# Optimization experiments

Measured on AMD Instinct MI355X. Metric: run time of the kernel, lower is better.

Reference implementation:

```python
import jax, jax.numpy as jnp
import numpy as np

NEG_SLOPE = 0.2  # PyG GATConv default


def gat_conv(x, edge_index, W, a_src, a_dst, bias):
    """Single-head PyG-style GATConv (eval mode, add_self_loops=True)."""
    N = x.shape[0]
    h = x @ W  # [N, F_out]
    # add self loops
    loops = jnp.arange(N, dtype=edge_index.dtype)
    src = jnp.concatenate([edge_index[0], loops])  # [E+N]
    dst = jnp.concatenate([edge_index[1], loops])
    # per-edge attention logits: a_src . h_j + a_dst . h_i  (j=src, i=dst)
    alpha_s = h @ a_src  # [N]
    alpha_d = h @ a_dst  # [N]
    e = jax.nn.leaky_relu(alpha_s[src] + alpha_d[dst], NEG_SLOPE)  # [E+N]
    # segment softmax over incoming edges of each dst node
    m = jax.ops.segment_max(e, dst, num_segments=N)
    ex = jnp.exp(e - m[dst])
    denom = jax.ops.segment_sum(ex, dst, num_segments=N)
    alpha = ex / denom[dst]  # [E+N]
    # weighted scatter-aggregate of source features
    out = jax.ops.segment_sum(h[src] * alpha[:, None], dst, num_segments=N)
    return out + bias


def setup_inputs() -> dict:
    key = jax.random.key(0)
    ks = jax.random.split(key, 12)
    N, E = 100000, 3200000
    Fin, H, Fout = 128, 32, 32
    x = jax.random.normal(ks[0], (N, Fin), dtype=jnp.float32)
    edge_index = jax.random.randint(ks[1], (2, E), 0, N, dtype=jnp.int64)
    s = 1.0 / np.sqrt(Fin)
    W1 = jax.random.uniform(ks[2], (Fin, H), jnp.float32, -s, s)
    a1s = jax.random.uniform(ks[3], (H,), jnp.float32, -s, s)
    a1d = jax.random.uniform(ks[4], (H,), jnp.float32, -s, s)
    b1 = jnp.zeros((H,), jnp.float32)
    s2 = 1.0 / np.sqrt(H)
    W2 = jax.random.uniform(ks[5], (H, H), jnp.float32, -s2, s2)
    a2s = jax.random.uniform(ks[6], (H,), jnp.float32, -s2, s2)
    a2d = jax.random.uniform(ks[7], (H,), jnp.float32, -s2, s2)
    b2 = jnp.zeros((H,), jnp.float32)
    Wf = jax.random.uniform(ks[8], (H, Fout), jnp.float32, -s2, s2)
    bf = jax.random.uniform(ks[9], (Fout,), jnp.float32, -s2, s2)
    return {"x": x, "edge_index": edge_index, "W1": W1, "a1s": a1s, "a1d": a1d,
            "b1": b1, "W2": W2, "a2s": a2s, "a2d": a2d, "b2": b2,
            "Wf": Wf, "bf": bf}


def reference(x, edge_index, W1, a1s, a1d, b1, W2, a2s, a2d, b2, Wf, bf):
    h = jax.nn.relu(gat_conv(x, edge_index, W1, a1s, a1d, b1))
    h = jax.nn.relu(gat_conv(h, edge_index, W2, a2s, a2d, b2))
    return h @ Wf + bf
```

## Files before the change

### kernel.cpp

```cpp
#include <hip/hip_runtime.h>

#define NEG_SLOPE 0.2f
#define BK_LOG 9
#define BK_NODES (1 << BK_LOG)
#define TILE_EPT 24
#define TILE_E (256 * TILE_EPT)

typedef __attribute__((ext_vector_type(8))) short bf8_t;
typedef __attribute__((ext_vector_type(4))) float f32x4;

__device__ __forceinline__ float leaky(float v) { return v > 0.0f ? v : NEG_SLOPE * v; }

__device__ __forceinline__ unsigned short f2bf(float f) {
    unsigned u = __float_as_uint(f);
    u += 0x7fffu + ((u >> 16) & 1u);
    return (unsigned short)(u >> 16);
}
__device__ __forceinline__ float bf2f(unsigned short h) {
    return __uint_as_float(((unsigned)h) << 16);
}

__device__ __forceinline__ int scan256_excl(int v, int* tmp) {
    int t = threadIdx.x;
    tmp[t] = v;
    __syncthreads();
    for (int d = 1; d < 256; d <<= 1) {
        int x = (t >= d) ? tmp[t - d] : 0;
        __syncthreads();
        tmp[t] += x;
        __syncthreads();
    }
    int r = tmp[t] - v;
    __syncthreads();
    return r;
}

__device__ __forceinline__ void wsplit_body(int blk, int tid,
                                            const float* __restrict__ W,
                                            unsigned short* __restrict__ wh,
                                            unsigned short* __restrict__ wl, int K) {
    int idx = blk * 256 + tid;
    int KT = K >> 5;
    if (idx >= KT * 128) return;
    int lane = idx & 63;
    int nt = (idx >> 6) & 1;
    int kt = idx >> 7;
    int q = lane >> 4, c = lane & 15;
#pragma unroll
    for (int j = 0; j < 8; ++j) {
        int k = kt * 32 + q * 8 + j;
        int n = nt * 16 + c;
        float w = W[k * 32 + n];
        unsigned short hi = f2bf(w);
        wh[idx * 8 + j] = hi;
        wl[idx * 8 + j] = f2bf(w - bf2f(hi));
    }
}

__global__ __launch_bounds__(256) void k_prep(
    const float* __restrict__ W1, unsigned short* __restrict__ wh1, unsigned short* __restrict__ wl1,
    int* __restrict__ bcnt)
{
    int b = blockIdx.x, t = threadIdx.x;
    if (b < 2) wsplit_body(b, t, W1, wh1, wl1, 128);
    else       bcnt[t] = 0;
}

template <int FIN>
__device__ __forceinline__ void gemm_body(
    int blk, int tid,
    const float* __restrict__ x,
    const unsigned short* __restrict__ wh, const unsigned short* __restrict__ wl,
    const float* __restrict__ a_s, const float* __restrict__ a_d,
    float* __restrict__ h, float* __restrict__ alpha_s,
    float* __restrict__ alpha_d, int N)
{
    constexpr int KT = FIN / 32;
    int lane = tid & 63;
    int mt   = blk * 4 + (tid >> 6);
    int m0   = mt * 16;
    if (m0 >= N) return;
    int q = lane >> 4, c = lane & 15;

    bf8_t Bh[KT][2], Bl[KT][2];
#pragma unroll
    for (int kt = 0; kt < KT; ++kt)
#pragma unroll
        for (int nt = 0; nt < 2; ++nt) {
            Bh[kt][nt] = *(const bf8_t*)(wh + ((size_t)(kt * 2 + nt) * 64 + lane) * 8);
            Bl[kt][nt] = *(const bf8_t*)(wl + ((size_t)(kt * 2 + nt) * 64 + lane) * 8);
        }

    int rowa = m0 + c;
    if (rowa >= N) rowa = N - 1;
    const float* xr = x + (size_t)rowa * FIN;
    bf8_t Ah[KT], Al[KT];
#pragma unroll
    for (int kt = 0; kt < KT; ++kt) {
        f32x4 v0 = *(const f32x4*)(xr + kt * 32 + q * 8);
        f32x4 v1 = *(const f32x4*)(xr + kt * 32 + q * 8 + 4);
#pragma unroll
        for (int j = 0; j < 8; ++j) {
            float f = (j < 4) ? v0[j] : v1[j - 4];
            unsigned short hi = f2bf(f);
            Ah[kt][j] = (short)hi;
            Al[kt][j] = (short)f2bf(f - bf2f(hi));
        }
    }

    f32x4 acc0 = {0.f, 0.f, 0.f, 0.f}, acc1 = {0.f, 0.f, 0.f, 0.f};
#pragma unroll
    for (int kt = 0; kt < KT; ++kt) {
        acc0 = __builtin_amdgcn_mfma_f32_16x16x32_bf16(Ah[kt], Bh[kt][0], acc0, 0, 0, 0);
        acc1 = __builtin_amdgcn_mfma_f32_16x16x32_bf16(Ah[kt], Bh[kt][1], acc1, 0, 0, 0);
        acc0 = __builtin_amdgcn_mfma_f32_16x16x32_bf16(Al[kt], Bh[kt][0], acc0, 0, 0, 0);
        acc1 = __builtin_amdgcn_mfma_f32_16x16x32_bf16(Al[kt], Bh[kt][1], acc1, 0, 0, 0);
        acc0 = __builtin_amdgcn_mfma_f32_16x16x32_bf16(Ah[kt], Bl[kt][0], acc0, 0, 0, 0);
        acc1 = __builtin_amdgcn_mfma_f32_16x16x32_bf16(Ah[kt], Bl[kt][1], acc1, 0, 0, 0);
    }

#pragma unroll
    for (int reg = 0; reg < 4; ++reg) {
        int r = m0 + q * 4 + reg;
        if (r < N) {
            h[(size_t)r * 32 + c]      = acc0[reg];
            h[(size_t)r * 32 + 16 + c] = acc1[reg];
        }
    }
    float as0 = a_s[c], as1 = a_s[c + 16];
    float ad0 = a_d[c], ad1 = a_d[c + 16];
#pragma unroll
    for (int reg = 0; reg < 4; ++reg) {
        float ps = acc0[reg] * as0 + acc1[reg] * as1;
        float pd = acc0[reg] * ad0 + acc1[reg] * ad1;
#pragma unroll
        for (int msk = 8; msk >= 1; msk >>= 1) {
            ps += __shfl_xor(ps, msk);
            pd += __shfl_xor(pd, msk);
        }
        int r = m0 + q * 4 + reg;
        if (c == 0 && r < N) {
            alpha_s[r] = ps;
            alpha_d[r] = pd;
        }
    }
}

__global__ __launch_bounds__(256) void k_bcount_gemm1(
    const int* __restrict__ edst, int* __restrict__ bcnt, int E, int nb_tile,
    const float* __restrict__ x,
    const unsigned short* __restrict__ wh, const unsigned short* __restrict__ wl,
    const float* __restrict__ a_s, const float* __restrict__ a_d,
    float* __restrict__ h, float* __restrict__ alpha_s,
    float* __restrict__ alpha_d, int N)
{
    if ((int)blockIdx.x < nb_tile) {
        __shared__ int th[256];
        int t = threadIdx.x;
        th[t] = 0;
        __syncthreads();
        int base = blockIdx.x * TILE_E;
        int rem  = min(TILE_E, E - base);
        if ((E & 3) == 0) {
            const int4* ed4 = (const int4*)(edst + base);
            int nv = rem >> 2;
            for (int k = t; k < nv; k += 256) {
                int4 d = ed4[k];
                atomicAdd(&th[d.x >> BK_LOG], 1);
                atomicAdd(&th[d.y >> BK_LOG], 1);
                atomicAdd(&th[d.z >> BK_LOG], 1);
                atomicAdd(&th[d.w >> BK_LOG], 1);
            }
            for (int e = (nv << 2) + t; e < rem; e += 256)
                atomicAdd(&th[edst[base + e] >> BK_LOG], 1);
        } else {
            for (int e = t; e < rem; e += 256)
                atomicAdd(&th[edst[base + e] >> BK_LOG], 1);
        }
        __syncthreads();
        if (th[t]) atomicAdd(&bcnt[t], th[t]);
    } else {
        gemm_body<128>(blockIdx.x - nb_tile, threadIdx.x, x, wh, wl,
                       a_s, a_d, h, alpha_s, alpha_d, N);
    }
}


__global__ __launch_bounds__(256) void k_bscan(const int* __restrict__ bcnt,
                                               int* __restrict__ bbase,
                                               int* __restrict__ bcur,
                                               int* __restrict__ off, int N, int E) {
    __shared__ int tmp[256];
    int t = threadIdx.x;
    int ex = scan256_excl(bcnt[t], tmp);
    bbase[t] = ex;
    bcur[t]  = ex;
    if (t == 0) { bbase[256] = E; off[N] = E; }
}

__global__ __launch_bounds__(256) void k_bplace(const int* __restrict__ esrc,
                                                const int* __restrict__ edst,
                                                int* __restrict__ bcur,
                                                unsigned* __restrict__ pairs, int E) {
    __shared__ int th[256], rb[256];
    int t = threadIdx.x;
    th[t] = 0;
    __syncthreads();
    int base = blockIdx.x * TILE_E;
    int rem  = min(TILE_E, E - base);
    bool vec = ((E & 3) == 0);
    if (vec) {
        const int4* ed4 = (const int4*)(edst + base);
        int nv = rem >> 2;
        for (int k = t; k < nv; k += 256) {
            int4 d = ed4[k];
            atomicAdd(&th[d.x >> BK_LOG], 1);
            atomicAdd(&th[d.y >> BK_LOG], 1);
            atomicAdd(&th[d.z >> BK_LOG], 1);
            atomicAdd(&th[d.w >> BK_LOG], 1);
        }
        for (int e = (nv << 2) + t; e < rem; e += 256)
            atomicAdd(&th[edst[base + e] >> BK_LOG], 1);
    } else {
        for (int e = t; e < rem; e += 256)
            atomicAdd(&th[edst[base + e] >> BK_LOG], 1);
    }
    __syncthreads();
    int cnt = th[t];
    if (cnt) rb[t] = atomicAdd(&bcur[t], cnt);
    th[t] = 0;
    __syncthreads();
    if (vec) {
        const int4* ed4 = (const int4*)(edst + base);
        const int4* es4 = (const int4*)(esrc + base);
        int nv = rem >> 2;
        for (int k = t; k < nv; k += 256) {
            int4 d = ed4[k];
            int4 s = es4[k];
            int b0 = d.x >> BK_LOG, r0 = atomicAdd(&th[b0], 1);
            pairs[rb[b0] + r0] = ((unsigned)s.x << BK_LOG) | (unsigned)(d.x & (BK_NODES - 1));
            int b1 = d.y >> BK_LOG, r1 = atomicAdd(&th[b1], 1);
            pairs[rb[b1] + r1] = ((unsigned)s.y << BK_LOG) | (unsigned)(d.y & (BK_NODES - 1));
            int b2 = d.z >> BK_LOG, r2 = atomicAdd(&th[b2], 1);
            pairs[rb[b2] + r2] = ((unsigned)s.z << BK_LOG) | (unsigned)(d.z & (BK_NODES - 1));
            int b3 = d.w >> BK_LOG, r3 = atomicAdd(&th[b3], 1);
            pairs[rb[b3] + r3] = ((unsigned)s.w << BK_LOG) | (unsigned)(d.w & (BK_NODES - 1));
        }
        for (int e = (nv << 2) + t; e < rem; e += 256) {
            int d = edst[base + e], s = esrc[base + e];
            int b = d >> BK_LOG, r = atomicAdd(&th[b], 1);
            pairs[rb[b] + r] = ((unsigned)s << BK_LOG) | (unsigned)(d & (BK_NODES - 1));
        }
    } else {
        for (int e = t; e < rem; e += 256) {
            int d = edst[base + e], s = esrc[base + e];
            int b = d >> BK_LOG, r = atomicAdd(&th[b], 1);
            pairs[rb[b] + r] = ((unsigned)s << BK_LOG) | (unsigned)(d & (BK_NODES - 1));
        }
    }
}

__global__ __launch_bounds__(512) void k_csr(const int* __restrict__ bbase,
                                             const unsigned* __restrict__ pairs,
                                             int* __restrict__ off,
                                             int* __restrict__ csr, int N) {
    __shared__ int lh[BK_NODES], lx[BK_NODES];
    int b = blockIdx.x, t = threadIdx.x;
    int lo = bbase[b], hi = bbase[b + 1];
    int node0 = b << BK_LOG;
    lh[t] = 0;
    __syncthreads();
    for (int j = lo + t; j < hi; j += 512)
        atomicAdd(&lh[pairs[j] & (BK_NODES - 1)], 1);
    __syncthreads();
    lx[t] = lh[t];
    __syncthreads();
    for (int d = 1; d < BK_NODES; d <<= 1) {
        int x0 = (t >= d) ? lx[t - d] : 0;
        __syncthreads();
        lx[t] += x0;
        __syncthreads();
    }
    lx[t] -= lh[t];
    if (node0 + t < N) off[node0 + t] = lo + lx[t];
    lh[t] = 0;
    __syncthreads();
    for (int j = lo + t; j < hi; j += 512) {
        unsigned p  = pairs[j];
        int      li = p & (BK_NODES - 1);
        int      r  = atomicAdd(&lh[li], 1);
        csr[lo + lx[li] + r] = (int)(p >> BK_LOG);
    }
}

template <bool FINAL>
__global__ __launch_bounds__(256) void fused_agg(
    const int* __restrict__ csr, const int* __restrict__ off,
    const float* __restrict__ alpha_s, const float* __restrict__ alpha_d,
    const float* __restrict__ h, const float* __restrict__ bias,
    const float* __restrict__ Wn,
    const float* __restrict__ an_s, const float* __restrict__ an_d,
    const float* __restrict__ bn,
    float* __restrict__ outh,
    float* __restrict__ out_as, float* __restrict__ out_ad, int N)
{
    int t = blockIdx.x * 256 + threadIdx.x;
    int i = t >> 3, q = t & 7;
    if (i >= N) return;
    int s0 = off[i], s1 = off[i + 1];
    float ad = alpha_d[i];

    const float* hq = h + q * 4;

    float w   = __expf(leaky(alpha_s[i] + ad));
    float den = w;
    f32x4 hv  = *(const f32x4*)(hq + (size_t)i * 32);
    f32x4 acc;
    acc[0] = w * hv[0]; acc[1] = w * hv[1]; acc[2] = w * hv[2]; acc[3] = w * hv[3];

    for (int j = s0; j < s1; j += 32) {
        int i0 = j + q, i1 = i0 + 8, i2 = i0 + 16, i3 = i0 + 24;
        int c0 = (i0 < s1) ? csr[i0] : 0;
        int c1 = (i1 < s1) ? csr[i1] : 0;
        int c2 = (i2 < s1) ? csr[i2] : 0;
        int c3 = (i3 < s1) ? csr[i3] : 0;
        float e0x = __expf(leaky(alpha_s[c0] + ad));
        float e1x = __expf(leaky(alpha_s[c1] + ad));
        float e2x = __expf(leaky(alpha_s[c2] + ad));
        float e3x = __expf(leaky(alpha_s[c3] + ad));
        float w0 = (i0 < s1) ? e0x : 0.0f;
        float w1 = (i1 < s1) ? e1x : 0.0f;
        float w2 = (i2 < s1) ? e2x : 0.0f;
        float w3 = (i3 < s1) ? e3x : 0.0f;
        int o0 = c0 << 5, o1 = c1 << 5, o2 = c2 << 5, o3 = c3 << 5;
#pragma unroll
        for (int e = 0; e < 8; ++e) {
            int   e0 = __shfl(o0, e, 8); float f0 = __shfl(w0, e, 8);
            int   e1 = __shfl(o1, e, 8); float f1 = __shfl(w1, e, 8);
            int   e2 = __shfl(o2, e, 8); float f2 = __shfl(w2, e, 8);
            int   e3 = __shfl(o3, e, 8); float f3 = __shfl(w3, e, 8);
            f32x4 g0 = *(const f32x4*)(hq + e0);
            f32x4 g1 = *(const f32x4*)(hq + e1);
            f32x4 g2 = *(const f32x4*)(hq + e2);
            f32x4 g3 = *(const f32x4*)(hq + e3);
            den += (f0 + f1) + (f2 + f3);
            acc[0] += f0 * g0[0]; acc[1] += f0 * g0[1];
            acc[2] += f0 * g0[2]; acc[3] += f0 * g0[3];
            acc[0] += f1 * g1[0]; acc[1] += f1 * g1[1];
            acc[2] += f1 * g1[2]; acc[3] += f1 * g1[3];
            acc[0] += f2 * g2[0]; acc[1] += f2 * g2[1];
            acc[2] += f2 * g2[2]; acc[3] += f2 * g2[3];
            acc[0] += f3 * g3[0]; acc[1] += f3 * g3[1];
            acc[2] += f3 * g3[2]; acc[3] += f3 * g3[3];
        }
    }

    float inv = 1.0f / den;
    f32x4 b4  = *(const f32x4*)(bias + q * 4);
    f32x4 r;
    r[0] = fmaxf(acc[0] * inv + b4[0], 0.0f);
    r[1] = fmaxf(acc[1] * inv + b4[1], 0.0f);
    r[2] = fmaxf(acc[2] * inv + b4[2], 0.0f);
    r[3] = fmaxf(acc[3] * inv + b4[3], 0.0f);

    f32x4 m = {0.f, 0.f, 0.f, 0.f};
#pragma unroll
    for (int e = 0; e < 8; ++e) {
        f32x4 rv;
        rv[0] = __shfl(r[0], e, 8);
        rv[1] = __shfl(r[1], e, 8);
        rv[2] = __shfl(r[2], e, 8);
        rv[3] = __shfl(r[3], e, 8);
#pragma unroll
        for (int jj = 0; jj < 4; ++jj) {
            f32x4 wr = *(const f32x4*)(Wn + (e * 4 + jj) * 32 + q * 4);
            m[0] += rv[jj] * wr[0]; m[1] += rv[jj] * wr[1];
            m[2] += rv[jj] * wr[2]; m[3] += rv[jj] * wr[3];
        }
    }

    if (FINAL) {
        f32x4 bb = *(const f32x4*)(bn + q * 4);
        m[0] += bb[0]; m[1] += bb[1]; m[2] += bb[2]; m[3] += bb[3];
        *(f32x4*)(outh + (size_t)i * 32 + q * 4) = m;
    } else {
        *(f32x4*)(outh + (size_t)i * 32 + q * 4) = m;
        f32x4 as4 = *(const f32x4*)(an_s + q * 4);
        f32x4 ad4 = *(const f32x4*)(an_d + q * 4);
        float ps = m[0] * as4[0] + m[1] * as4[1] + m[2] * as4[2] + m[3] * as4[3];
        float pd = m[0] * ad4[0] + m[1] * ad4[1] + m[2] * ad4[2] + m[3] * ad4[3];
#pragma unroll
        for (int msk = 4; msk >= 1; msk >>= 1) {
            ps += __shfl_xor(ps, msk, 8);
            pd += __shfl_xor(pd, msk, 8);
        }
        if (q == 0) { out_as[i] = ps; out_ad[i] = pd; }
    }
}

extern "C" void kernel_launch(void* const* d_in, const int* in_sizes, int n_in,
                              void* d_out, int out_size, void* d_ws, size_t ws_size,
                              hipStream_t stream)
{
    const float* x   = (const float*)d_in[0];
    const int*   ei  = (const int*)d_in[1];
    const float* W1  = (const float*)d_in[2];
    const float* a1s = (const float*)d_in[3];
    const float* a1d = (const float*)d_in[4];
    const float* b1  = (const float*)d_in[5];
    const float* W2  = (const float*)d_in[6];
    const float* a2s = (const float*)d_in[7];
    const float* a2d = (const float*)d_in[8];
    const float* b2  = (const float*)d_in[9];
    const float* Wf  = (const float*)d_in[10];
    const float* bf  = (const float*)d_in[11];

    const int N = in_sizes[0] / 128;
    const int E = in_sizes[1] / 2;
    const int* esrc = ei;
    const int* edst = ei + E;
    const int B1 = (N + BK_NODES - 1) >> BK_LOG;

    float* ws = (float*)d_ws;
    float* h1       = ws;
    float* h2       = h1 + (size_t)N * 32;
    float* alpha_s  = h2 + (size_t)N * 32;
    float* alpha_d  = alpha_s + N;
    float* alpha_s2 = alpha_d + N;
    float* alpha_d2 = alpha_s2 + N;
    int*   off      = (int*)(alpha_d2 + N);
    int*   csr      = off + (N + 1);
    int*   bcnt     = csr + E;
    int*   bbase    = bcnt + 256;
    int*   bcur     = bbase + 257;
    unsigned short* wfb =
        (unsigned short*)(((uintptr_t)(bcur + 256) + 15) & ~(uintptr_t)15);
    unsigned short* wh1 = wfb;
    unsigned short* wl1 = wh1 + 4096;
    unsigned* pairs = ((size_t)E <= (size_t)32 * N)
                          ? (unsigned*)h2
                          : (unsigned*)(wl1 + 4096);

    const int nb_agg  = (N * 8 + 255) / 256;
    const int nb_tile = (E + TILE_E - 1) / TILE_E;
    const int nb_gemm = ((N + 15) / 16 + 3) / 4;

    k_prep<<<3, 256, 0, stream>>>(W1, wh1, wl1, bcnt);

    k_bcount_gemm1<<<nb_tile + nb_gemm, 256, 0, stream>>>(
        edst, bcnt, E, nb_tile, x, wh1, wl1, a1s, a1d, h1, alpha_s, alpha_d, N);

    k_bscan  <<<1, 256, 0, stream>>>(bcnt, bbase, bcur, off, N, E);
    k_bplace <<<nb_tile, 256, 0, stream>>>(esrc, edst, bcur, pairs, E);
    k_csr    <<<B1, 512, 0, stream>>>(bbase, pairs, off, csr, N);

    fused_agg<false><<<nb_agg, 256, 0, stream>>>(
        csr, off, alpha_s, alpha_d, h1, b1, W2, a2s, a2d, nullptr,
        h2, alpha_s2, alpha_d2, N);

    fused_agg<true><<<nb_agg, 256, 0, stream>>>(
        csr, off, alpha_s2, alpha_d2, h2, b2, Wf, nullptr, nullptr, bf,
        (float*)d_out, nullptr, nullptr, N);
}
```

Before: 342.9 us.

## Precompute per-edge exp weights in CSR build and vectorize aggregation loads

The unnormalized attention weight exp(leaky(alpha_s[src]+alpha_d[dst])) is now computed per edge and stored in a wexp array, during CSR construction for layer 1 and in a separate k_wexp2 kernel for layer 2. The aggregation kernels read it with aligned int4/float4 loads of csr and wexp instead of gathering alpha_s per edge and shuffling indices within lane groups. Bucket size is halved to 256 nodes, giving 512 buckets, so k_csr runs 256-thread blocks and keeps alpha_d in shared memory. This trades an extra E-sized float write/read and an extra kernel launch for fewer scattered gathers and shuffles in the aggregation loop. Each lane now walks the whole edge list of its node redundantly, rather than splitting it across the 8 lanes.

```diff
diff --git a/kernel.cpp b/kernel.cpp
--- a/kernel.cpp
+++ b/kernel.cpp
@@ -1,8 +1,9 @@
 #include <hip/hip_runtime.h>
 
 #define NEG_SLOPE 0.2f
-#define BK_LOG 9
+#define BK_LOG 8
 #define BK_NODES (1 << BK_LOG)
+#define NBK 512
 #define TILE_EPT 24
 #define TILE_E (256 * TILE_EPT)
 
@@ -18,21 +19,6 @@
 }
 __device__ __forceinline__ float bf2f(unsigned short h) {
     return __uint_as_float(((unsigned)h) << 16);
-}
-
-__device__ __forceinline__ int scan256_excl(int v, int* tmp) {
-    int t = threadIdx.x;
-    tmp[t] = v;
-    __syncthreads();
-    for (int d = 1; d < 256; d <<= 1) {
-        int x = (t >= d) ? tmp[t - d] : 0;
-        __syncthreads();
-        tmp[t] += x;
-        __syncthreads();
-    }
-    int r = tmp[t] - v;
-    __syncthreads();
-    return r;
 }
 
 __device__ __forceinline__ void wsplit_body(int blk, int tid,
@@ -63,7 +49,7 @@
 {
     int b = blockIdx.x, t = threadIdx.x;
     if (b < 2) wsplit_body(b, t, W1, wh1, wl1, 128);
-    else       bcnt[t] = 0;
+    else       { bcnt[t] = 0; bcnt[t + 256] = 0; }
 }
 
 template <int FIN>
@@ -155,9 +141,9 @@
     float* __restrict__ alpha_d, int N)
 {
     if ((int)blockIdx.x < nb_tile) {
-        __shared__ int th[256];
+        __shared__ int th[NBK];
         int t = threadIdx.x;
-        th[t] = 0;
+        th[t] = 0; th[t + 256] = 0;
         __syncthreads();
         int base = blockIdx.x * TILE_E;
         int rem  = min(TILE_E, E - base);
@@ -178,7 +164,8 @@
                 atomicAdd(&th[edst[base + e] >> BK_LOG], 1);
         }
         __syncthreads();
-        if (th[t]) atomicAdd(&bcnt[t], th[t]);
+        if (th[t])       atomicAdd(&bcnt[t], th[t]);
+        if (th[t + 256]) atomicAdd(&bcnt[t + 256], th[t + 256]);
     } else {
         gemm_body<128>(blockIdx.x - nb_tile, threadIdx.x, x, wh, wl,
                        a_s, a_d, h, alpha_s, alpha_d, N);
@@ -186,25 +173,38 @@
 }
 
 
-__global__ __launch_bounds__(256) void k_bscan(const int* __restrict__ bcnt,
+__global__ __launch_bounds__(512) void k_bscan(const int* __restrict__ bcnt,
                                                int* __restrict__ bbase,
                                                int* __restrict__ bcur,
-                                               int* __restrict__ off, int N, int E) {
-    __shared__ int tmp[256];
+                                               int* __restrict__ off,
+                                               int* __restrict__ csr,
+                                               float* __restrict__ wexp,
+                                               int N, int E) {
+    __shared__ int tmp[NBK];
     int t = threadIdx.x;
-    int ex = scan256_excl(bcnt[t], tmp);
+    int v = bcnt[t];
+    tmp[t] = v;
+    __syncthreads();
+    for (int d = 1; d < NBK; d <<= 1) {
+        int x = (t >= d) ? tmp[t - d] : 0;
+        __syncthreads();
+        tmp[t] += x;
+        __syncthreads();
+    }
+    int ex = tmp[t] - v;
     bbase[t] = ex;
     bcur[t]  = ex;
-    if (t == 0) { bbase[256] = E; off[N] = E; }
+    if (t == 0) { bbase[NBK] = E; off[N] = E; }
+    if (t < 32) { csr[E + t] = 0; wexp[E + t] = 0.0f; }
 }
 
 __global__ __launch_bounds__(256) void k_bplace(const int* __restrict__ esrc,
                                                 const int* __restrict__ edst,
                                                 int* __restrict__ bcur,
                                                 unsigned* __restrict__ pairs, int E) {
-    __shared__ int th[256], rb[256];
+    __shared__ int th[NBK], rb[NBK];
     int t = threadIdx.x;
-    th[t] = 0;
+    th[t] = 0; th[t + 256] = 0;
     __syncthreads();
     int base = blockIdx.x * TILE_E;
     int rem  = min(TILE_E, E - base);
@@ -226,9 +226,9 @@
             atomicAdd(&th[edst[base + e] >> BK_LOG], 1);
     }
     __syncthreads();
-    int cnt = th[t];
-    if (cnt) rb[t] = atomicAdd(&bcur[t], cnt);
-    th[t] = 0;
+    if (th[t])       rb[t]       = atomicAdd(&bcur[t],       th[t]);
+    if (th[t + 256]) rb[t + 256] = atomicAdd(&bcur[t + 256], th[t + 256]);
+    th[t] = 0; th[t + 256] = 0;
     __syncthreads();
     if (vec) {
         const int4* ed4 = (const int4*)(edst + base);
@@ -260,17 +260,22 @@
     }
 }
 
-__global__ __launch_bounds__(512) void k_csr(const int* __restrict__ bbase,
+__global__ __launch_bounds__(256) void k_csr(const int* __restrict__ bbase,
                                              const unsigned* __restrict__ pairs,
+                                             const float* __restrict__ alpha_s,
+                                             const float* __restrict__ alpha_d,
                                              int* __restrict__ off,
-                                             int* __restrict__ csr, int N) {
+                                             int* __restrict__ csr,
+                                             float* __restrict__ wexp, int N) {
     __shared__ int lh[BK_NODES], lx[BK_NODES];
+    __shared__ float adL[BK_NODES];
     int b = blockIdx.x, t = threadIdx.x;
     int lo = bbase[b], hi = bbase[b + 1];
     int node0 = b << BK_LOG;
+    adL[t] = (node0 + t < N) ? alpha_d[node0 + t] : 0.0f;
     lh[t] = 0;
     __syncthreads();
-    for (int j = lo + t; j < hi; j += 512)
+    for (int j = lo + t; j < hi; j += 256)
         atomicAdd(&lh[pairs[j] & (BK_NODES - 1)], 1);
     __syncthreads();
     lx[t] = lh[t];
@@ -285,17 +290,35 @@
     if (node0 + t < N) off[node0 + t] = lo + lx[t];
     lh[t] = 0;
     __syncthreads();
-    for (int j = lo + t; j < hi; j += 512) {
+    for (int j = lo + t; j < hi; j += 256) {
         unsigned p  = pairs[j];
         int      li = p & (BK_NODES - 1);
+        int      s  = (int)(p >> BK_LOG);
         int      r  = atomicAdd(&lh[li], 1);
-        csr[lo + lx[li] + r] = (int)(p >> BK_LOG);
-    }
+        int      pos = lo + lx[li] + r;
+        csr[pos]  = s;
+        wexp[pos] = __expf(leaky(alpha_s[s] + adL[li]));
+    }
+}
+
+__global__ __launch_bounds__(256) void k_wexp2(
+    const int* __restrict__ csr, const int* __restrict__ off,
+    const float* __restrict__ alpha_s, const float* __restrict__ alpha_d,
+    float* __restrict__ wexp, int N)
+{
+    int t = blockIdx.x * 256 + threadIdx.x;
+    int i = t >> 3, q = t & 7;
+    if (i >= N) return;
+    int s0 = off[i], s1 = off[i + 1];
+    float ad = alpha_d[i];
+    for (int j = s0 + q; j < s1; j += 8)
+        wexp[j] = __expf(leaky(alpha_s[csr[j]] + ad));
 }
 
 template <bool FINAL>
 __global__ __launch_bounds__(256) void fused_agg(
     const int* __restrict__ csr, const int* __restrict__ off,
+    const float* __restrict__ wexp,
     const float* __restrict__ alpha_s, const float* __restrict__ alpha_d,
     const float* __restrict__ h, const float* __restrict__ bias,
     const float* __restrict__ Wn,
@@ -308,50 +331,33 @@
     int i = t >> 3, q = t & 7;
     if (i >= N) return;
     int s0 = off[i], s1 = off[i + 1];
-    float ad = alpha_d[i];
+    int deg = s1 - s0;
 
     const float* hq = h + q * 4;
 
-    float w   = __expf(leaky(alpha_s[i] + ad));
+    float w   = __expf(leaky(alpha_s[i] + alpha_d[i]));
     float den = w;
     f32x4 hv  = *(const f32x4*)(hq + (size_t)i * 32);
     f32x4 acc;
     acc[0] = w * hv[0]; acc[1] = w * hv[1]; acc[2] = w * hv[2]; acc[3] = w * hv[3];
 
-    for (int j = s0; j < s1; j += 32) {
-        int i0 = j + q, i1 = i0 + 8, i2 = i0 + 16, i3 = i0 + 24;
-        int c0 = (i0 < s1) ? csr[i0] : 0;
-        int c1 = (i1 < s1) ? csr[i1] : 0;
-        int c2 = (i2 < s1) ? csr[i2] : 0;
-        int c3 = (i3 < s1) ? csr[i3] : 0;
-        float e0x = __expf(leaky(alpha_s[c0] + ad));
-        float e1x = __expf(leaky(alpha_s[c1] + ad));
-        float e2x = __expf(leaky(alpha_s[c2] + ad));
-        float e3x = __expf(leaky(alpha_s[c3] + ad));
-        float w0 = (i0 < s1) ? e0x : 0.0f;
-        float w1 = (i1 < s1) ? e1x : 0.0f;
-        float w2 = (i2 < s1) ? e2x : 0.0f;
-        float w3 = (i3 < s1) ? e3x : 0.0f;
-        int o0 = c0 << 5, o1 = c1 << 5, o2 = c2 << 5, o3 = c3 << 5;
-#pragma unroll
-        for (int e = 0; e < 8; ++e) {
-            int   e0 = __shfl(o0, e, 8); float f0 = __shfl(w0, e, 8);
-            int   e1 = __shfl(o1, e, 8); float f1 = __shfl(w1, e, 8);
-            int   e2 = __shfl(o2, e, 8); float f2 = __shfl(w2, e, 8);
-            int   e3 = __shfl(o3, e, 8); float f3 = __shfl(w3, e, 8);
-            f32x4 g0 = *(const f32x4*)(hq + e0);
-            f32x4 g1 = *(const f32x4*)(hq + e1);
-            f32x4 g2 = *(const f32x4*)(hq + e2);
-            f32x4 g3 = *(const f32x4*)(hq + e3);
-            den += (f0 + f1) + (f2 + f3);
-            acc[0] += f0 * g0[0]; acc[1] += f0 * g0[1];
-            acc[2] += f0 * g0[2]; acc[3] += f0 * g0[3];
-            acc[0] += f1 * g1[0]; acc[1] += f1 * g1[1];
-            acc[2] += f1 * g1[2]; acc[3] += f1 * g1[3];
-            acc[0] += f2 * g2[0]; acc[1] += f2 * g2[1];
-            acc[2] += f2 * g2[2]; acc[3] += f2 * g2[3];
-            acc[0] += f3 * g3[0]; acc[1] += f3 * g3[1];
-            acc[2] += f3 * g3[2]; acc[3] += f3 * g3[3];
+    for (int j = s0 & ~31; j < s1; j += 32) {
+        const int4*  c4 = (const int4*)(csr + j);
+        const f32x4* w4 = (const f32x4*)(wexp + j);
+        int rel0 = j - s0;
+#pragma unroll
+        for (int r = 0; r < 8; ++r) {
+            int4  ci = c4[r];
+            f32x4 wi = w4[r];
+#pragma unroll
+            for (int k = 0; k < 4; ++k) {
+                float we = ((unsigned)(rel0 + r * 4 + k) < (unsigned)deg) ? wi[k] : 0.0f;
+                int   ce = (k == 0) ? ci.x : (k == 1) ? ci.y : (k == 2) ? ci.z : ci.w;
+                f32x4 g  = *(const f32x4*)(hq + (ce << 5));
+                den += we;
+                acc[0] += we * g[0]; acc[1] += we * g[1];
+                acc[2] += we * g[2]; acc[3] += we * g[3];
+            }
         }
     }
 
@@ -429,12 +435,13 @@
     float* alpha_s2 = alpha_d + N;
     float* alpha_d2 = alpha_s2 + N;
     int*   off      = (int*)(alpha_d2 + N);
-    int*   csr      = off + (N + 1);
-    int*   bcnt     = csr + E;
-    int*   bbase    = bcnt + 256;
-    int*   bcur     = bbase + 257;
+    int*   csr      = off + (N + 8);
+    float* wexp     = (float*)(csr + (E + 32));
+    int*   bcnt     = (int*)(wexp + (E + 32));
+    int*   bbase    = bcnt + NBK;
+    int*   bcur     = bbase + (NBK + 1);
     unsigned short* wfb =
-        (unsigned short*)(((uintptr_t)(bcur + 256) + 15) & ~(uintptr_t)15);
+        (unsigned short*)(((uintptr_t)(bcur + NBK) + 15) & ~(uintptr_t)15);
     unsigned short* wh1 = wfb;
     unsigned short* wl1 = wh1 + 4096;
     unsigned* pairs = ((size_t)E <= (size_t)32 * N)
@@ -450,15 +457,18 @@
     k_bcount_gemm1<<<nb_tile + nb_gemm, 256, 0, stream>>>(
         edst, bcnt, E, nb_tile, x, wh1, wl1, a1s, a1d, h1, alpha_s, alpha_d, N);
 
-    k_bscan  <<<1, 256, 0, stream>>>(bcnt, bbase, bcur, off, N, E);
+    k_bscan  <<<1, NBK, 0, stream>>>(bcnt, bbase, bcur, off, csr, wexp, N, E);
     k_bplace <<<nb_tile, 256, 0, stream>>>(esrc, edst, bcur, pairs, E);
-    k_csr    <<<B1, 512, 0, stream>>>(bbase, pairs, off, csr, N);
+    k_csr    <<<B1, 256, 0, stream>>>(bbase, pairs, alpha_s, alpha_d,
+                                      off, csr, wexp, N);
 
     fused_agg<false><<<nb_agg, 256, 0, stream>>>(
-        csr, off, alpha_s, alpha_d, h1, b1, W2, a2s, a2d, nullptr,
+        csr, off, wexp, alpha_s, alpha_d, h1, b1, W2, a2s, a2d, nullptr,
         h2, alpha_s2, alpha_d2, N);
 
+    k_wexp2<<<nb_agg, 256, 0, stream>>>(csr, off, alpha_s2, alpha_d2, wexp, N);
+
     fused_agg<true><<<nb_agg, 256, 0, stream>>>(
-        csr, off, alpha_s2, alpha_d2, h2, b2, Wf, nullptr, nullptr, bf,
+        csr, off, wexp, alpha_s2, alpha_d2, h2, b2, Wf, nullptr, nullptr, bf,
         (float*)d_out, nullptr, nullptr, N);
 }
```

Result: slower. 468.7 us (+36.7%).

## Place edges into fixed-capacity buckets in one pass, dropping count and scan kernels

Applied to the files above, without the earlier changes.

Edges are now scattered directly into per-bucket regions of fixed capacity (average bucket size plus slack), so the separate global bucket-count pass, the single-block scan kernel and the second edge read are gone. The bucket-offset prefix scan moves into each k_csr block, which reads from the padded bucket region. This removes one full read of edst and two kernel launches. The risk is overflow if a bucket exceeds capacity on skewed graphs, and the workspace layout is rearranged so pairs can alias h2.

```diff
diff --git a/kernel.cpp b/kernel.cpp
--- a/kernel.cpp
+++ b/kernel.cpp
@@ -18,21 +18,6 @@
 }
 __device__ __forceinline__ float bf2f(unsigned short h) {
     return __uint_as_float(((unsigned)h) << 16);
-}
-
-__device__ __forceinline__ int scan256_excl(int v, int* tmp) {
-    int t = threadIdx.x;
-    tmp[t] = v;
-    __syncthreads();
-    for (int d = 1; d < 256; d <<= 1) {
-        int x = (t >= d) ? tmp[t - d] : 0;
-        __syncthreads();
-        tmp[t] += x;
-        __syncthreads();
-    }
-    int r = tmp[t] - v;
-    __syncthreads();
-    return r;
 }
 
 __device__ __forceinline__ void wsplit_body(int blk, int tid,
@@ -58,12 +43,16 @@
 }
 
 __global__ __launch_bounds__(256) void k_prep(
-    const float* __restrict__ W1, unsigned short* __restrict__ wh1, unsigned short* __restrict__ wl1,
-    int* __restrict__ bcnt)
+    const float* __restrict__ W1, unsigned short* __restrict__ wh1,
+    unsigned short* __restrict__ wl1,
+    int* __restrict__ bcur, int* __restrict__ off, int N, int E)
 {
     int b = blockIdx.x, t = threadIdx.x;
     if (b < 2) wsplit_body(b, t, W1, wh1, wl1, 128);
-    else       bcnt[t] = 0;
+    else {
+        bcur[t] = 0;
+        if (t == 0) off[N] = E;
+    }
 }
 
 template <int FIN>
@@ -146,8 +135,10 @@
     }
 }
 
-__global__ __launch_bounds__(256) void k_bcount_gemm1(
-    const int* __restrict__ edst, int* __restrict__ bcnt, int E, int nb_tile,
+__global__ __launch_bounds__(256) void k_place_gemm1(
+    const int* __restrict__ esrc, const int* __restrict__ edst,
+    int* __restrict__ bcur, unsigned* __restrict__ pairs,
+    int E, int cap, int nb_tile,
     const float* __restrict__ x,
     const unsigned short* __restrict__ wh, const unsigned short* __restrict__ wl,
     const float* __restrict__ a_s, const float* __restrict__ a_d,
@@ -155,13 +146,14 @@
     float* __restrict__ alpha_d, int N)
 {
     if ((int)blockIdx.x < nb_tile) {
-        __shared__ int th[256];
+        __shared__ int th[256], rb[256];
         int t = threadIdx.x;
         th[t] = 0;
         __syncthreads();
         int base = blockIdx.x * TILE_E;
         int rem  = min(TILE_E, E - base);
-        if ((E & 3) == 0) {
+        bool vec = ((E & 3) == 0);
+        if (vec) {
             const int4* ed4 = (const int4*)(edst + base);
             int nv = rem >> 2;
             for (int k = t; k < nv; k += 256) {
@@ -178,100 +170,73 @@
                 atomicAdd(&th[edst[base + e] >> BK_LOG], 1);
         }
         __syncthreads();
-        if (th[t]) atomicAdd(&bcnt[t], th[t]);
+        if (th[t]) rb[t] = atomicAdd(&bcur[t], th[t]);
+        th[t] = 0;
+        __syncthreads();
+        if (vec) {
+            const int4* ed4 = (const int4*)(edst + base);
+            const int4* es4 = (const int4*)(esrc + base);
+            int nv = rem >> 2;
+            for (int k = t; k < nv; k += 256) {
+                int4 d = ed4[k];
+                int4 s = es4[k];
+                int b0 = d.x >> BK_LOG, r0 = atomicAdd(&th[b0], 1);
+                pairs[(size_t)b0 * cap + rb[b0] + r0] =
+                    ((unsigned)s.x << BK_LOG) | (unsigned)(d.x & (BK_NODES - 1));
+                int b1 = d.y >> BK_LOG, r1 = atomicAdd(&th[b1], 1);
+                pairs[(size_t)b1 * cap + rb[b1] + r1] =
+                    ((unsigned)s.y << BK_LOG) | (unsigned)(d.y & (BK_NODES - 1));
+                int b2 = d.z >> BK_LOG, r2 = atomicAdd(&th[b2], 1);
+                pairs[(size_t)b2 * cap + rb[b2] + r2] =
+                    ((unsigned)s.z << BK_LOG) | (unsigned)(d.z & (BK_NODES - 1));
+                int b3 = d.w >> BK_LOG, r3 = atomicAdd(&th[b3], 1);
+                pairs[(size_t)b3 * cap + rb[b3] + r3] =
+                    ((unsigned)s.w << BK_LOG) | (unsigned)(d.w & (BK_NODES - 1));
+            }
+            for (int e = (nv << 2) + t; e < rem; e += 256) {
+                int d = edst[base + e], s = esrc[base + e];
+                int b = d >> BK_LOG, r = atomicAdd(&th[b], 1);
+                pairs[(size_t)b * cap + rb[b] + r] =
+                    ((unsigned)s << BK_LOG) | (unsigned)(d & (BK_NODES - 1));
+            }
+        } else {
+            for (int e = t; e < rem; e += 256) {
+                int d = edst[base + e], s = esrc[base + e];
+                int b = d >> BK_LOG, r = atomicAdd(&th[b], 1);
+                pairs[(size_t)b * cap + rb[b] + r] =
+                    ((unsigned)s << BK_LOG) | (unsigned)(d & (BK_NODES - 1));
+            }
+        }
     } else {
         gemm_body<128>(blockIdx.x - nb_tile, threadIdx.x, x, wh, wl,
                        a_s, a_d, h, alpha_s, alpha_d, N);
     }
 }
 
-
-__global__ __launch_bounds__(256) void k_bscan(const int* __restrict__ bcnt,
-                                               int* __restrict__ bbase,
-                                               int* __restrict__ bcur,
-                                               int* __restrict__ off, int N, int E) {
-    __shared__ int tmp[256];
-    int t = threadIdx.x;
-    int ex = scan256_excl(bcnt[t], tmp);
-    bbase[t] = ex;
-    bcur[t]  = ex;
-    if (t == 0) { bbase[256] = E; off[N] = E; }
-}
-
-__global__ __launch_bounds__(256) void k_bplace(const int* __restrict__ esrc,
-                                                const int* __restrict__ edst,
-                                                int* __restrict__ bcur,
-                                                unsigned* __restrict__ pairs, int E) {
-    __shared__ int th[256], rb[256];
-    int t = threadIdx.x;
-    th[t] = 0;
-    __syncthreads();
-    int base = blockIdx.x * TILE_E;
-    int rem  = min(TILE_E, E - base);
-    bool vec = ((E & 3) == 0);
-    if (vec) {
-        const int4* ed4 = (const int4*)(edst + base);
-        int nv = rem >> 2;
-        for (int k = t; k < nv; k += 256) {
-            int4 d = ed4[k];
-            atomicAdd(&th[d.x >> BK_LOG], 1);
-            atomicAdd(&th[d.y >> BK_LOG], 1);
-            atomicAdd(&th[d.z >> BK_LOG], 1);
-            atomicAdd(&th[d.w >> BK_LOG], 1);
-        }
-        for (int e = (nv << 2) + t; e < rem; e += 256)
-            atomicAdd(&th[edst[base + e] >> BK_LOG], 1);
-    } else {
-        for (int e = t; e < rem; e += 256)
-            atomicAdd(&th[edst[base + e] >> BK_LOG], 1);
-    }
-    __syncthreads();
-    int cnt = th[t];
-    if (cnt) rb[t] = atomicAdd(&bcur[t], cnt);
-    th[t] = 0;
-    __syncthreads();
-    if (vec) {
-        const int4* ed4 = (const int4*)(edst + base);
-        const int4* es4 = (const int4*)(esrc + base);
-        int nv = rem >> 2;
-        for (int k = t; k < nv; k += 256) {
-            int4 d = ed4[k];
-            int4 s = es4[k];
-            int b0 = d.x >> BK_LOG, r0 = atomicAdd(&th[b0], 1);
-            pairs[rb[b0] + r0] = ((unsigned)s.x << BK_LOG) | (unsigned)(d.x & (BK_NODES - 1));
-            int b1 = d.y >> BK_LOG, r1 = atomicAdd(&th[b1], 1);
-            pairs[rb[b1] + r1] = ((unsigned)s.y << BK_LOG) | (unsigned)(d.y & (BK_NODES - 1));
-            int b2 = d.z >> BK_LOG, r2 = atomicAdd(&th[b2], 1);
-            pairs[rb[b2] + r2] = ((unsigned)s.z << BK_LOG) | (unsigned)(d.z & (BK_NODES - 1));
-            int b3 = d.w >> BK_LOG, r3 = atomicAdd(&th[b3], 1);
-            pairs[rb[b3] + r3] = ((unsigned)s.w << BK_LOG) | (unsigned)(d.w & (BK_NODES - 1));
-        }
-        for (int e = (nv << 2) + t; e < rem; e += 256) {
-            int d = edst[base + e], s = esrc[base + e];
-            int b = d >> BK_LOG, r = atomicAdd(&th[b], 1);
-            pairs[rb[b] + r] = ((unsigned)s << BK_LOG) | (unsigned)(d & (BK_NODES - 1));
-        }
-    } else {
-        for (int e = t; e < rem; e += 256) {
-            int d = edst[base + e], s = esrc[base + e];
-            int b = d >> BK_LOG, r = atomicAdd(&th[b], 1);
-            pairs[rb[b] + r] = ((unsigned)s << BK_LOG) | (unsigned)(d & (BK_NODES - 1));
-        }
-    }
-}
-
-__global__ __launch_bounds__(512) void k_csr(const int* __restrict__ bbase,
+__global__ __launch_bounds__(512) void k_csr(const int* __restrict__ bcur,
                                              const unsigned* __restrict__ pairs,
                                              int* __restrict__ off,
-                                             int* __restrict__ csr, int N) {
-    __shared__ int lh[BK_NODES], lx[BK_NODES];
+                                             int* __restrict__ csr,
+                                             int cap, int nbk, int N) {
+    __shared__ int lh[BK_NODES], lx[BK_NODES], bs[256];
     int b = blockIdx.x, t = threadIdx.x;
-    int lo = bbase[b], hi = bbase[b + 1];
+    if (t < 256) bs[t] = (t < nbk) ? bcur[t] : 0;
+    __syncthreads();
+    for (int d = 1; d < 256; d <<= 1) {
+        int v = 0;
+        if (t < 256 && t >= d) v = bs[t - d];
+        __syncthreads();
+        if (t < 256) bs[t] += v;
+        __syncthreads();
+    }
+    int lo  = (b > 0) ? bs[b - 1] : 0;
+    int cnt = bcur[b];
+    const unsigned* bp = pairs + (size_t)b * cap;
     int node0 = b << BK_LOG;
     lh[t] = 0;
     __syncthreads();
-    for (int j = lo + t; j < hi; j += 512)
-        atomicAdd(&lh[pairs[j] & (BK_NODES - 1)], 1);
+    for (int j = t; j < cnt; j += 512)
+        atomicAdd(&lh[bp[j] & (BK_NODES - 1)], 1);
     __syncthreads();
     lx[t] = lh[t];
     __syncthreads();
@@ -285,8 +250,8 @@
     if (node0 + t < N) off[node0 + t] = lo + lx[t];
     lh[t] = 0;
     __syncthreads();
-    for (int j = lo + t; j < hi; j += 512) {
-        unsigned p  = pairs[j];
+    for (int j = t; j < cnt; j += 512) {
+        unsigned p  = bp[j];
         int      li = p & (BK_NODES - 1);
         int      r  = atomicAdd(&lh[li], 1);
         csr[lo + lx[li] + r] = (int)(p >> BK_LOG);
@@ -419,25 +384,24 @@
     const int E = in_sizes[1] / 2;
     const int* esrc = ei;
     const int* edst = ei + E;
-    const int B1 = (N + BK_NODES - 1) >> BK_LOG;
+    const int NBK = (N + BK_NODES - 1) >> BK_LOG;
+    const int cap = (int)(((long long)E * BK_NODES + N - 1) / N) + 768;
 
     float* ws = (float*)d_ws;
     float* h1       = ws;
     float* h2       = h1 + (size_t)N * 32;
-    float* alpha_s  = h2 + (size_t)N * 32;
+    float* alpha_s2 = h2 + (size_t)N * 32;
+    float* alpha_d2 = alpha_s2 + N;
+    float* alpha_s  = alpha_d2 + N;
     float* alpha_d  = alpha_s + N;
-    float* alpha_s2 = alpha_d + N;
-    float* alpha_d2 = alpha_s2 + N;
-    int*   off      = (int*)(alpha_d2 + N);
-    int*   csr      = off + (N + 1);
-    int*   bcnt     = csr + E;
-    int*   bbase    = bcnt + 256;
-    int*   bcur     = bbase + 257;
+    int*   off      = (int*)(alpha_d + N);
+    int*   csr      = off + (N + 8);
+    int*   bcur     = csr + (E + 8);
     unsigned short* wfb =
         (unsigned short*)(((uintptr_t)(bcur + 256) + 15) & ~(uintptr_t)15);
     unsigned short* wh1 = wfb;
     unsigned short* wl1 = wh1 + 4096;
-    unsigned* pairs = ((size_t)E <= (size_t)32 * N)
+    unsigned* pairs = ((size_t)NBK * cap <= (size_t)N * 34)
                           ? (unsigned*)h2
                           : (unsigned*)(wl1 + 4096);
 
@@ -445,14 +409,13 @@
     const int nb_tile = (E + TILE_E - 1) / TILE_E;
     const int nb_gemm = ((N + 15) / 16 + 3) / 4;
 
-    k_prep<<<3, 256, 0, stream>>>(W1, wh1, wl1, bcnt);
-
-    k_bcount_gemm1<<<nb_tile + nb_gemm, 256, 0, stream>>>(
-        edst, bcnt, E, nb_tile, x, wh1, wl1, a1s, a1d, h1, alpha_s, alpha_d, N);
-
-    k_bscan  <<<1, 256, 0, stream>>>(bcnt, bbase, bcur, off, N, E);
-    k_bplace <<<nb_tile, 256, 0, stream>>>(esrc, edst, bcur, pairs, E);
-    k_csr    <<<B1, 512, 0, stream>>>(bbase, pairs, off, csr, N);
+    k_prep<<<3, 256, 0, stream>>>(W1, wh1, wl1, bcur, off, N, E);
+
+    k_place_gemm1<<<nb_tile + nb_gemm, 256, 0, stream>>>(
+        esrc, edst, bcur, pairs, E, cap, nb_tile,
+        x, wh1, wl1, a1s, a1d, h1, alpha_s, alpha_d, N);
+
+    k_csr<<<NBK, 512, 0, stream>>>(bcur, pairs, off, csr, cap, NBK, N);
 
     fused_agg<false><<<nb_agg, 256, 0, stream>>>(
         csr, off, alpha_s, alpha_d, h1, b1, W2, a2s, a2d, nullptr,
```

New measurement: 313.5 us. -8.6%, faster.
